# Optimization experiments

Measured on AMD Instinct MI355X. Metric: run time of the kernel, lower is better.

Reference implementation:

```python
import jax, jax.numpy as jnp
import numpy as np

H, HK, HD, WIN = 16, 4, 128, 512  # query heads, kv heads, head_dim, window
NEG = -1e30


def setup_inputs() -> dict:
    key = jax.random.key(0)
    ks = jax.random.split(key, 5)
    B, T, D = 2, 4096, 2048
    s = 1.0 / np.sqrt(D)
    return {
        "x": jax.random.normal(ks[0], (B, T, D), dtype=jnp.float32),
        "Wq": jax.random.normal(ks[1], (D, H * HD), dtype=jnp.float32) * s,
        "Wk": jax.random.normal(ks[2], (D, HK * HD), dtype=jnp.float32) * s,
        "Wv": jax.random.normal(ks[3], (D, HK * HD), dtype=jnp.float32) * s,
        "Wo": jax.random.normal(ks[4], (H * HD, D), dtype=jnp.float32) * s,
    }


def _local_attn(x, Wq, Wk, Wv, Wo):
    B, T, D = x.shape
    nrep = H // HK
    nb = T // WIN
    scale = 1.0 / np.sqrt(HD)

    q = (x @ Wq).reshape(B, nb, WIN, HK, nrep, HD)
    k = (x @ Wk).reshape(B, nb, WIN, HK, HD)
    v = (x @ Wv).reshape(B, nb, WIN, HK, HD)

    # each query block attends to its own block + the previous block,
    k_prev = jnp.concatenate([jnp.zeros_like(k[:, :1]), k[:, :-1]], axis=1)
    v_prev = jnp.concatenate([jnp.zeros_like(v[:, :1]), v[:, :-1]], axis=1)
    kcat = jnp.concatenate([k_prev, k], axis=2)  # [B,nb,2W,HK,HD]
    vcat = jnp.concatenate([v_prev, v], axis=2)

    r = jnp.arange(WIN)[:, None]       # query offset in block
    c = jnp.arange(2 * WIN)[None, :]   # key offset in concat window
    allowed = jnp.where(c < WIN, c > r, (c - WIN) <= r)  # [W,2W]
    first_block = (jnp.arange(nb) == 0)[:, None, None]   # block 0 has no prev
    allowed = allowed[None, :, :] & ~(first_block & (c < WIN)[None])  # [nb,W,2W]

    scores = jnp.einsum('bnqhrd,bnkhd->bnhrqk', q, kcat) * scale
    scores = jnp.where(allowed[None, :, None, None], scores, NEG)
    attn = jax.nn.softmax(scores, axis=-1)
    out = jnp.einsum('bnhrqk,bnkhd->bnqhrd', attn, vcat)
    out = out.reshape(B, T, H * HD)
    return out @ Wo


def reference(x, Wq, Wk, Wv, Wo):
    return _local_attn(x, Wq, Wk, Wv, Wo)
```

## Files before the change

kernel.cpp:

```cpp
#include <hip/hip_runtime.h>
#include <stdint.h>


typedef unsigned short u16;
typedef __attribute__((ext_vector_type(8))) short frag8;
typedef __attribute__((ext_vector_type(4))) float f32x4;

#define TILE 128

__device__ __forceinline__ u16 f2bf(float f) {
  union { float f; unsigned u; } c; c.f = f;
  unsigned u = c.u;
  return (u16)((u + 0x7fffu + ((u >> 16) & 1u)) >> 16);
}

__device__ __forceinline__ void async16(const u16* g, u16* l) {
  __builtin_amdgcn_global_load_lds((const __attribute__((address_space(1))) void*)g,
                                   (__attribute__((address_space(3))) void*)l, 16, 0, 0);
}

__device__ __forceinline__ void xcd_map(int& bx, int& by) {
  const int gx = gridDim.x;
  const int cx = gx >> 3;
  int id = blockIdx.y * gx + blockIdx.x;
  int xcd = id & 7, local = id >> 3;
  bx = xcd * cx + (local % cx);
  by = local / cx;
}

template <typename OutT>
__global__ __launch_bounds__(512, 2) void k_gemm256(const u16* __restrict__ A, int lda,
                                                    const u16* __restrict__ Bt, int ldb,
                                                    OutT* __restrict__ C, int ldc, int K,
                                                    float oscale) {
  __shared__ alignas(16) u16 Ab[2][256 * 64];
  __shared__ alignas(16) u16 Bb[2][256 * 64];
  const int tid = threadIdx.x, lane = tid & 63, wave = tid >> 6;
  const int wm = wave >> 2, wn = wave & 3;
  const int quad = lane >> 4, l16 = lane & 15;

  int bx, by;
  xcd_map(bx, by);

  const int rsub = wave * 8 + (lane >> 3);
  const int csub = ((lane & 7) ^ (lane >> 3)) * 8;
  const u16* Ag = A + ((long)bx * 256 + rsub) * lda + csub;
  const u16* Bg = Bt + ((long)by * 256 + rsub) * ldb + csub;
  const long a64 = (long)64 * lda, b64 = (long)64 * ldb;

  const int rsw = (l16 & 7) << 3;

  f32x4 acc[8][4];
#pragma unroll
  for (int i = 0; i < 8; ++i)
#pragma unroll
    for (int j = 0; j < 4; ++j) acc[i][j] = (f32x4){0.f, 0.f, 0.f, 0.f};

  const int nt = K >> 6;

#pragma unroll
  for (int c = 0; c < 4; ++c) {
    async16(Ag + c * a64, &Ab[0][c * 4096 + wave * 512]);
    async16(Bg + c * b64, &Bb[0][c * 4096 + wave * 512]);
  }

  for (int t = 0; t < nt; ++t) {
    const int buf = t & 1, nb = buf ^ 1;
    const long koff = (long)(t + 1) << 6;
    frag8 af[4][2], bf[2][2];

    if (t + 1 < nt) {
#pragma unroll
      for (int c = 0; c < 4; ++c) {
        async16(Ag + c * a64 + koff, &Ab[nb][c * 4096 + wave * 512]);
        async16(Bg + c * b64 + koff, &Bb[nb][c * 4096 + wave * 512]);
      }
      asm volatile("s_waitcnt vmcnt(8)" ::: "memory");
    } else {
      asm volatile("s_waitcnt vmcnt(0)" ::: "memory");
    }
    __builtin_amdgcn_s_barrier();
    asm volatile("" ::: "memory");

#pragma unroll
    for (int i = 0; i < 4; ++i)
#pragma unroll
      for (int kk = 0; kk < 2; ++kk)
        af[i][kk] = *(const frag8*)(&Ab[buf][(wm * 128 + i * 16 + l16) * 64 +
                                             ((kk * 32 + quad * 8) ^ rsw)]);
#pragma unroll
    for (int j = 0; j < 2; ++j)
#pragma unroll
      for (int kk = 0; kk < 2; ++kk)
        bf[j][kk] = *(const frag8*)(&Bb[buf][(wn * 64 + j * 16 + l16) * 64 +
                                             ((kk * 32 + quad * 8) ^ rsw)]);
    __builtin_amdgcn_s_setprio(1);
#pragma unroll
    for (int kk = 0; kk < 2; ++kk)
#pragma unroll
      for (int i = 0; i < 4; ++i)
#pragma unroll
        for (int j = 0; j < 2; ++j)
          acc[i][j] = __builtin_amdgcn_mfma_f32_16x16x32_bf16(af[i][kk], bf[j][kk], acc[i][j], 0, 0, 0);
    __builtin_amdgcn_s_setprio(0);
    __builtin_amdgcn_s_barrier();

#pragma unroll
    for (int j = 0; j < 2; ++j)
#pragma unroll
      for (int kk = 0; kk < 2; ++kk)
        bf[j][kk] = *(const frag8*)(&Bb[buf][(wn * 64 + (j + 2) * 16 + l16) * 64 +
                                             ((kk * 32 + quad * 8) ^ rsw)]);
    __builtin_amdgcn_s_setprio(1);
#pragma unroll
    for (int kk = 0; kk < 2; ++kk)
#pragma unroll
      for (int i = 0; i < 4; ++i)
#pragma unroll
        for (int j = 0; j < 2; ++j)
          acc[i][j + 2] = __builtin_amdgcn_mfma_f32_16x16x32_bf16(af[i][kk], bf[j][kk], acc[i][j + 2], 0, 0, 0);
    __builtin_amdgcn_s_setprio(0);
    __builtin_amdgcn_s_barrier();

#pragma unroll
    for (int i = 0; i < 4; ++i)
#pragma unroll
      for (int kk = 0; kk < 2; ++kk)
        af[i][kk] = *(const frag8*)(&Ab[buf][(wm * 128 + (i + 4) * 16 + l16) * 64 +
                                             ((kk * 32 + quad * 8) ^ rsw)]);
#pragma unroll
    for (int j = 0; j < 2; ++j)
#pragma unroll
      for (int kk = 0; kk < 2; ++kk)
        bf[j][kk] = *(const frag8*)(&Bb[buf][(wn * 64 + j * 16 + l16) * 64 +
                                             ((kk * 32 + quad * 8) ^ rsw)]);
    __builtin_amdgcn_s_setprio(1);
#pragma unroll
    for (int kk = 0; kk < 2; ++kk)
#pragma unroll
      for (int i = 0; i < 4; ++i)
#pragma unroll
        for (int j = 0; j < 2; ++j)
          acc[i + 4][j] = __builtin_amdgcn_mfma_f32_16x16x32_bf16(af[i][kk], bf[j][kk], acc[i + 4][j], 0, 0, 0);
    __builtin_amdgcn_s_setprio(0);
    __builtin_amdgcn_s_barrier();

#pragma unroll
    for (int j = 0; j < 2; ++j)
#pragma unroll
      for (int kk = 0; kk < 2; ++kk)
        bf[j][kk] = *(const frag8*)(&Bb[buf][(wn * 64 + (j + 2) * 16 + l16) * 64 +
                                             ((kk * 32 + quad * 8) ^ rsw)]);
    __builtin_amdgcn_s_setprio(1);
#pragma unroll
    for (int kk = 0; kk < 2; ++kk)
#pragma unroll
      for (int i = 0; i < 4; ++i)
#pragma unroll
        for (int j = 0; j < 2; ++j)
          acc[i + 4][j + 2] = __builtin_amdgcn_mfma_f32_16x16x32_bf16(af[i][kk], bf[j][kk], acc[i + 4][j + 2], 0, 0, 0);
    __builtin_amdgcn_s_setprio(0);
    __builtin_amdgcn_s_barrier();
  }

  OutT* Ct = C + ((long)bx * 256 + wm * 128) * ldc + (long)by * 256 + wn * 64;
#pragma unroll
  for (int i = 0; i < 8; ++i)
#pragma unroll
    for (int j = 0; j < 4; ++j) {
      int r0 = i * 16 + quad * 4, cc = j * 16 + l16;
#pragma unroll
      for (int r = 0; r < 4; ++r) {
        float v = acc[i][j][r] * oscale;
        if constexpr (sizeof(OutT) == 2)
          Ct[(long)(r0 + r) * ldc + cc] = f2bf(v);
        else
          Ct[(long)(r0 + r) * ldc + cc] = v;
      }
    }
}

__device__ __forceinline__ void gemm_core(const u16* __restrict__ A, int lda,
                                          const u16* __restrict__ Bt, int ldb,
                                          int K, u16* As, u16* Bs, f32x4 acc[4][4]) {
  const int tid = threadIdx.x;
  const int lane = tid & 63, wave = tid >> 6;
  const int wr = wave >> 1, wc = wave & 1;
  const int quad = lane >> 4, l16 = lane & 15;
#pragma unroll
  for (int i = 0; i < 4; ++i)
#pragma unroll
    for (int j = 0; j < 4; ++j) acc[i][j] = (f32x4){0.f, 0.f, 0.f, 0.f};

  const int row0 = tid >> 2, offc = (tid & 3) * 8;
  const int nt = K >> 5;

#pragma unroll
  for (int r = 0; r < 2; ++r) {
    int row = r * 64 + row0;
    async16(A + (long)row * lda + offc, As + r * 2048 + wave * 512);
    async16(Bt + (long)row * ldb + offc, Bs + r * 2048 + wave * 512);
  }

  for (int t = 0; t < nt; ++t) {
    const int bo = (t & 1) * 4096, nbo = bo ^ 4096;
    if (t + 1 < nt) {
      const int k0 = (t + 1) * 32;
#pragma unroll
      for (int r = 0; r < 2; ++r) {
        int row = r * 64 + row0;
        async16(A + (long)row * lda + k0 + offc, As + nbo + r * 2048 + wave * 512);
        async16(Bt + (long)row * ldb + k0 + offc, Bs + nbo + r * 2048 + wave * 512);
      }
      asm volatile("s_waitcnt vmcnt(4)" ::: "memory");
    } else {
      asm volatile("s_waitcnt vmcnt(0)" ::: "memory");
    }
    __builtin_amdgcn_s_barrier();
    asm volatile("" ::: "memory");

    frag8 af[4], bf[4];
#pragma unroll
    for (int i = 0; i < 4; ++i)
      af[i] = *(const frag8*)(As + bo + (wr * 64 + i * 16 + l16) * 32 + quad * 8);
#pragma unroll
    for (int j = 0; j < 4; ++j)
      bf[j] = *(const frag8*)(Bs + bo + (wc * 64 + j * 16 + l16) * 32 + quad * 8);
#pragma unroll
    for (int i = 0; i < 4; ++i)
#pragma unroll
      for (int j = 0; j < 4; ++j)
        acc[i][j] = __builtin_amdgcn_mfma_f32_16x16x32_bf16(af[i], bf[j], acc[i][j], 0, 0, 0);
    asm volatile("" ::: "memory");
    __builtin_amdgcn_s_barrier();
  }
}

#define EPI_COORDS                                             \
  const int lane = threadIdx.x & 63, wave = threadIdx.x >> 6;  \
  const int wr = wave >> 1, wc = wave & 1;                     \
  const int quad = lane >> 4, l16 = lane & 15;

__global__ __launch_bounds__(256) void k_gemm_bf16(const u16* __restrict__ A, int lda,
                                                   const u16* __restrict__ Bt, int ldb,
                                                   u16* __restrict__ C, int ldc, int K) {
  __shared__ alignas(16) u16 smem[4 * TILE * 32];
  int bx, by; xcd_map(bx, by);
  f32x4 acc[4][4];
  gemm_core(A + (long)bx * TILE * lda, lda,
            Bt + (long)by * TILE * ldb, ldb, K, smem, smem + 2 * TILE * 32, acc);
  EPI_COORDS
  u16* Ct = C + (long)bx * TILE * ldc + (long)by * TILE;
#pragma unroll
  for (int i = 0; i < 4; ++i)
#pragma unroll
    for (int j = 0; j < 4; ++j) {
      int r0 = wr * 64 + i * 16 + quad * 4, cc = wc * 64 + j * 16 + l16;
#pragma unroll
      for (int r = 0; r < 4; ++r) Ct[(long)(r0 + r) * ldc + cc] = f2bf(acc[i][j][r]);
    }
}

__global__ __launch_bounds__(256) void k_gemm_bf16t(const u16* __restrict__ A, int lda,
                                                    const u16* __restrict__ Bt, int ldb,
                                                    u16* __restrict__ Ct, int ldct, int K) {
  __shared__ alignas(16) u16 smem[4 * TILE * 32];
  int bx, by; xcd_map(bx, by);
  f32x4 acc[4][4];
  gemm_core(A + (long)bx * TILE * lda, lda,
            Bt + (long)by * TILE * ldb, ldb, K, smem, smem + 2 * TILE * 32, acc);
  EPI_COORDS
  u16* Cb = Ct + (long)by * TILE * ldct + (long)bx * TILE;
#pragma unroll
  for (int i = 0; i < 4; ++i)
#pragma unroll
    for (int j = 0; j < 4; ++j) {
      int n = wc * 64 + j * 16 + l16, m0 = wr * 64 + i * 16 + quad * 4;
      ushort4 o;
      o.x = f2bf(acc[i][j][0]); o.y = f2bf(acc[i][j][1]);
      o.z = f2bf(acc[i][j][2]); o.w = f2bf(acc[i][j][3]);
      *(ushort4*)(Cb + (long)n * ldct + m0) = o;
    }
}

__global__ __launch_bounds__(256, 2) void k_attn(const u16* __restrict__ qb,
                                                 const u16* __restrict__ kb,
                                                 const u16* __restrict__ vT,
                                                 u16* __restrict__ O) {
  __shared__ alignas(16) u16 Ks[2][64 * 128];
  __shared__ alignas(16) u16 Vs[2][128 * 64];
  const int tid = threadIdx.x, lane = tid & 63, wave = tid >> 6;
  const int quad = lane >> 4, l16 = lane & 15;

  const int id = blockIdx.x + 4 * blockIdx.y + 32 * blockIdx.z;
  const int g = (id & 7) | ((id >> 7) << 3);
  const int w = (id >> 3) & 15;
  const int hk = g & 3, blk = (g >> 2) & 7, b = g >> 5;
  const int h = hk * 4 + (w & 3), qi = w >> 2;

  const long tok_q = (long)b * 4096 + blk * 512 + qi * 128;

  frag8 qf[2][4];
#pragma unroll
  for (int i = 0; i < 2; ++i)
#pragma unroll
    for (int kt = 0; kt < 4; ++kt)
      qf[i][kt] = *(const frag8*)(qb + (tok_q + wave * 32 + i * 16 + l16) * 2048 +
                                  h * 128 + kt * 32 + quad * 8);

  f32x4 o_acc[2][8];
  float m_r[2][4], l_r[2][4];
#pragma unroll
  for (int i = 0; i < 2; ++i) {
#pragma unroll
    for (int j = 0; j < 8; ++j) o_acc[i][j] = (f32x4){0.f, 0.f, 0.f, 0.f};
#pragma unroll
    for (int r = 0; r < 4; ++r) { m_r[i][r] = -1e30f; l_r[i][r] = 0.f; }
  }

  const int rsw = (l16 & 7) << 3;

  auto stage = [&](int buf, int ci) {
    const long tk = (long)b * 4096 + (blk - 1) * 512 + ci * 64;
#pragma unroll
    for (int c = 0; c < 4; ++c) {
      const int idx = (wave * 4 + c) * 512 + lane * 8;
      {
        int row = idx >> 7, col = idx & 127;
        async16(kb + (tk + row) * 512 + hk * 128 + (col ^ ((row & 7) << 3)),
                &Ks[buf][(wave * 4 + c) * 512]);
      }
      {
        int row = idx >> 6, col = idx & 63;
        async16(vT + ((long)hk * 128 + row) * 8192 + tk + (col ^ ((row & 7) << 3)),
                &Vs[buf][(wave * 4 + c) * 512]);
      }
    }
  };

  const int c0 = blk ? 2 * qi : 8, c1 = 9 + 2 * qi;
  int cur = 0;
  stage(0, c0);
  asm volatile("s_waitcnt vmcnt(0)" ::: "memory");
  __builtin_amdgcn_s_barrier();
  asm volatile("" ::: "memory");

  for (int ci = c0; ci <= c1; ++ci) {
    if (ci < c1) stage(cur ^ 1, ci + 1);

    f32x4 s_acc[2][4];
#pragma unroll
    for (int i = 0; i < 2; ++i)
#pragma unroll
      for (int j = 0; j < 4; ++j) s_acc[i][j] = (f32x4){0.f, 0.f, 0.f, 0.f};
#pragma unroll
    for (int kt = 0; kt < 4; ++kt) {
      frag8 bfr[4];
#pragma unroll
      for (int j = 0; j < 4; ++j)
        bfr[j] = *(const frag8*)(&Ks[cur][(j * 16 + l16) * 128 + ((kt * 32 + quad * 8) ^ rsw)]);
#pragma unroll
      for (int i = 0; i < 2; ++i)
#pragma unroll
        for (int j = 0; j < 4; ++j)
          s_acc[i][j] = __builtin_amdgcn_mfma_f32_16x16x32_bf16(qf[i][kt], bfr[j], s_acc[i][j], 0, 0, 0);
    }

    const bool prev = (ci < 8);
    const int doff = (prev ? ci * 64 : (ci - 8) * 64) - qi * 128;
    float mc[2][4];
#pragma unroll
    for (int i = 0; i < 2; ++i)
#pragma unroll
      for (int r = 0; r < 4; ++r) mc[i][r] = -1e30f;
#pragma unroll
    for (int i = 0; i < 2; ++i)
#pragma unroll
      for (int j = 0; j < 4; ++j)
#pragma unroll
        for (int r = 0; r < 4; ++r) {
          int rl = wave * 32 + i * 16 + quad * 4 + r;
          int lk = j * 16 + l16;
          bool ok = prev ? (lk + doff > rl) : (lk + doff <= rl);
          float s = ok ? s_acc[i][j][r] : -1e30f;
          s_acc[i][j][r] = s;
          mc[i][r] = fmaxf(mc[i][r], s);
        }
#pragma unroll
    for (int o = 1; o < 16; o <<= 1)
#pragma unroll
      for (int i = 0; i < 2; ++i)
#pragma unroll
        for (int r = 0; r < 4; ++r)
          mc[i][r] = fmaxf(mc[i][r], __shfl_xor(mc[i][r], o));

    bool need = false;
#pragma unroll
    for (int i = 0; i < 2; ++i)
#pragma unroll
      for (int r = 0; r < 4; ++r) need = need || (mc[i][r] > m_r[i][r] + 8.f);
    if (__any(need)) {
      float alpha[2][4];
#pragma unroll
      for (int i = 0; i < 2; ++i)
#pragma unroll
        for (int r = 0; r < 4; ++r) {
          float mn = fmaxf(m_r[i][r], mc[i][r]);
          alpha[i][r] = __expf(m_r[i][r] - mn);
          m_r[i][r] = mn;
          l_r[i][r] *= alpha[i][r];
        }
#pragma unroll
      for (int i = 0; i < 2; ++i)
#pragma unroll
        for (int j = 0; j < 8; ++j)
#pragma unroll
          for (int r = 0; r < 4; ++r) o_acc[i][j][r] *= alpha[i][r];
    }

    float ps[2][4];
#pragma unroll
    for (int i = 0; i < 2; ++i)
#pragma unroll
      for (int r = 0; r < 4; ++r) ps[i][r] = 0.f;
#pragma unroll
    for (int i = 0; i < 2; ++i)
#pragma unroll
      for (int j = 0; j < 4; ++j)
#pragma unroll
        for (int r = 0; r < 4; ++r) {
          float s = s_acc[i][j][r];
          float e = __expf(s - m_r[i][r]);
          e = (s == -1e30f) ? 0.f : e;
          s_acc[i][j][r] = e;
          ps[i][r] += e;
        }
#pragma unroll
    for (int o = 1; o < 16; o <<= 1)
#pragma unroll
      for (int i = 0; i < 2; ++i)
#pragma unroll
        for (int r = 0; r < 4; ++r) ps[i][r] += __shfl_xor(ps[i][r], o);
#pragma unroll
    for (int i = 0; i < 2; ++i)
#pragma unroll
      for (int r = 0; r < 4; ++r) l_r[i][r] += ps[i][r];

    asm volatile("" ::: "memory");
    __builtin_amdgcn_s_barrier();
    asm volatile("" ::: "memory");

    u16* PsW = &Ks[cur][wave * 2048];
#pragma unroll
    for (int i = 0; i < 2; ++i)
#pragma unroll
      for (int r = 0; r < 4; ++r) {
        int xw = ((quad * 4 + r) & 7) << 3;
#pragma unroll
        for (int j = 0; j < 4; ++j)
          PsW[(i * 16 + quad * 4 + r) * 64 + ((j * 16 + l16) ^ xw)] = f2bf(s_acc[i][j][r]);
      }

#pragma unroll
    for (int kt = 0; kt < 2; ++kt) {
      frag8 pf[2], vf[8];
#pragma unroll
      for (int i = 0; i < 2; ++i)
        pf[i] = *(const frag8*)(PsW + (i * 16 + l16) * 64 + ((kt * 32 + quad * 8) ^ rsw));
#pragma unroll
      for (int j = 0; j < 8; ++j)
        vf[j] = *(const frag8*)(&Vs[cur][(j * 16 + l16) * 64 + ((kt * 32 + quad * 8) ^ rsw)]);
#pragma unroll
      for (int i = 0; i < 2; ++i)
#pragma unroll
        for (int j = 0; j < 8; ++j)
          o_acc[i][j] = __builtin_amdgcn_mfma_f32_16x16x32_bf16(pf[i], vf[j], o_acc[i][j], 0, 0, 0);
    }

    asm volatile("s_waitcnt vmcnt(0)" ::: "memory");
    __builtin_amdgcn_s_barrier();
    asm volatile("" ::: "memory");
    cur ^= 1;
  }

  float inv[2][4];
#pragma unroll
  for (int i = 0; i < 2; ++i)
#pragma unroll
    for (int r = 0; r < 4; ++r) inv[i][r] = 1.0f / l_r[i][r];
  u16* Ob = &Ks[0][0];
#pragma unroll
  for (int i = 0; i < 2; ++i)
#pragma unroll
    for (int j = 0; j < 8; ++j)
#pragma unroll
      for (int r = 0; r < 4; ++r)
        Ob[(wave * 32 + i * 16 + quad * 4 + r) * 128 + j * 16 + l16] =
            f2bf(o_acc[i][j][r] * inv[i][r]);
  __syncthreads();
#pragma unroll
  for (int p = 0; p < 8; ++p) {
    int idx = p * 256 + tid;
    int row = idx >> 4, col = (idx & 15) * 8;
    *(frag8*)(O + (tok_q + row) * 2048 + h * 128 + col) = *(const frag8*)(Ob + row * 128 + col);
  }
}

__global__ void k_convert(const float4* __restrict__ x, ushort4* __restrict__ xb) {
  int i = blockIdx.x * 256 + threadIdx.x;
  float4 f = x[i];
  ushort4 o;
  o.x = f2bf(f.x); o.y = f2bf(f.y); o.z = f2bf(f.z); o.w = f2bf(f.w);
  xb[i] = o;
}

__global__ void k_transpose(const float* __restrict__ W, u16* __restrict__ WT, int K, int N) {
  __shared__ float sh[32][33];
  int n0 = blockIdx.x * 32, k0 = blockIdx.y * 32;
  int tx = threadIdx.x, ty = threadIdx.y;
#pragma unroll
  for (int i = 0; i < 32; i += 8) sh[ty + i][tx] = W[(long)(k0 + ty + i) * N + n0 + tx];
  __syncthreads();
#pragma unroll
  for (int i = 0; i < 32; i += 8) WT[(long)(n0 + ty + i) * K + k0 + tx] = f2bf(sh[tx][ty + i]);
}

extern "C" void kernel_launch(void* const* d_in, const int* in_sizes, int n_in,
                              void* d_out, int out_size, void* d_ws, size_t ws_size,
                              hipStream_t stream) {
  const float* x  = (const float*)d_in[0];
  const float* Wq = (const float*)d_in[1];
  const float* Wk = (const float*)d_in[2];
  const float* Wv = (const float*)d_in[3];
  const float* Wo = (const float*)d_in[4];
  float* out = (float*)d_out;

  const long BT = 8192, D = 2048, NKV = 512;
  size_t off = 0;
  auto alloc = [&](size_t bytes) -> char* {
    off = (off + 255) & ~(size_t)255;
    char* p = (char*)d_ws + off;
    off += bytes;
    return p;
  };

  u16* xb  = (u16*)alloc((size_t)BT * D * 2);
  u16* WqT = (u16*)alloc((size_t)D * D * 2);
  u16* WkT = (u16*)alloc((size_t)NKV * D * 2);
  u16* WvT = (u16*)alloc((size_t)NKV * D * 2);
  u16* WoT = (u16*)alloc((size_t)D * D * 2);
  u16* qb  = (u16*)alloc((size_t)BT * D * 2);
  u16* kb  = (u16*)alloc((size_t)BT * NKV * 2);
  u16* vT  = (u16*)alloc((size_t)NKV * BT * 2);
  u16* Oa  = xb;

  k_convert<<<16384, 256, 0, stream>>>((const float4*)x, (ushort4*)xb);
  dim3 tb(32, 8);
  k_transpose<<<dim3(64, 64), tb, 0, stream>>>(Wq, WqT, 2048, 2048);
  k_transpose<<<dim3(16, 64), tb, 0, stream>>>(Wk, WkT, 2048, 512);
  k_transpose<<<dim3(16, 64), tb, 0, stream>>>(Wv, WvT, 2048, 512);
  k_transpose<<<dim3(64, 64), tb, 0, stream>>>(Wo, WoT, 2048, 2048);

  k_gemm256<u16><<<dim3(32, 8), 512, 0, stream>>>(xb, 2048, WqT, 2048, qb, 2048, 2048,
                                                  0.08838834764831845f);
  k_gemm_bf16 <<<dim3(64, 4),  256, 0, stream>>>(xb, 2048, WkT, 2048, kb, 512, 2048);
  k_gemm_bf16t<<<dim3(64, 4),  256, 0, stream>>>(xb, 2048, WvT, 2048, vT, 8192, 2048);

  k_attn<<<dim3(4, 8, 32), 256, 0, stream>>>(qb, kb, vT, Oa);

  k_gemm256<float><<<dim3(32, 8), 512, 0, stream>>>(Oa, 2048, WoT, 2048, out, 2048, 2048,
                                                    1.0f);
}
```

Measured before the change: 459.2 us.

## Single-buffer V tile, raise attention occupancy, skip unneeded masking, use exp2

The attention kernel keeps K double-buffered but gives V a single LDS buffer, loaded one iteration late. This frees LDS so launch bounds can go from two to three blocks per CU, and fine-grained vmcnt waits replace full drains. Masking is skipped for chunks that lie wholly inside the allowed region. Softmax uses raw v_exp_f32 (exp2), with log2(e) folded into the Q projection scale. The cost is extra barriers and tighter register budgets that could cause spills.

Result: slower. 545.2 us (+18.7%).

```diff
diff --git a/kernel.cpp b/kernel.cpp
--- a/kernel.cpp
+++ b/kernel.cpp
@@ -12,6 +12,12 @@
   union { float f; unsigned u; } c; c.f = f;
   unsigned u = c.u;
   return (u16)((u + 0x7fffu + ((u >> 16) & 1u)) >> 16);
+}
+
+__device__ __forceinline__ float fexp2(float x) {
+  float r;
+  asm("v_exp_f32 %0, %1" : "=v"(r) : "v"(x));
+  return r;
 }
 
 __device__ __forceinline__ void async16(const u16* g, u16* l) {
@@ -283,12 +289,12 @@
     }
 }
 
-__global__ __launch_bounds__(256, 2) void k_attn(const u16* __restrict__ qb,
+__global__ __launch_bounds__(256, 3) void k_attn(const u16* __restrict__ qb,
                                                  const u16* __restrict__ kb,
                                                  const u16* __restrict__ vT,
                                                  u16* __restrict__ O) {
   __shared__ alignas(16) u16 Ks[2][64 * 128];
-  __shared__ alignas(16) u16 Vs[2][128 * 64];
+  __shared__ alignas(16) u16 Vs[128 * 64];
   const int tid = threadIdx.x, lane = tid & 63, wave = tid >> 6;
   const int quad = lane >> 4, l16 = lane & 15;
 
@@ -320,33 +326,45 @@
 
   const int rsw = (l16 & 7) << 3;
 
-  auto stage = [&](int buf, int ci) {
+  auto stageK = [&](int buf, int ci) {
     const long tk = (long)b * 4096 + (blk - 1) * 512 + ci * 64;
 #pragma unroll
     for (int c = 0; c < 4; ++c) {
       const int idx = (wave * 4 + c) * 512 + lane * 8;
-      {
-        int row = idx >> 7, col = idx & 127;
-        async16(kb + (tk + row) * 512 + hk * 128 + (col ^ ((row & 7) << 3)),
-                &Ks[buf][(wave * 4 + c) * 512]);
-      }
-      {
-        int row = idx >> 6, col = idx & 63;
-        async16(vT + ((long)hk * 128 + row) * 8192 + tk + (col ^ ((row & 7) << 3)),
-                &Vs[buf][(wave * 4 + c) * 512]);
-      }
+      int row = idx >> 7, col = idx & 127;
+      async16(kb + (tk + row) * 512 + hk * 128 + (col ^ ((row & 7) << 3)),
+              &Ks[buf][(wave * 4 + c) * 512]);
+    }
+  };
+  auto stageV = [&](int ci) {
+    const long tk = (long)b * 4096 + (blk - 1) * 512 + ci * 64;
+#pragma unroll
+    for (int c = 0; c < 4; ++c) {
+      const int idx = (wave * 4 + c) * 512 + lane * 8;
+      int row = idx >> 6, col = idx & 63;
+      async16(vT + ((long)hk * 128 + row) * 8192 + tk + (col ^ ((row & 7) << 3)),
+              &Vs[(wave * 4 + c) * 512]);
     }
   };
 
   const int c0 = blk ? 2 * qi : 8, c1 = 9 + 2 * qi;
   int cur = 0;
-  stage(0, c0);
+  stageK(0, c0);
+  stageV(c0);
   asm volatile("s_waitcnt vmcnt(0)" ::: "memory");
   __builtin_amdgcn_s_barrier();
   asm volatile("" ::: "memory");
 
   for (int ci = c0; ci <= c1; ++ci) {
-    if (ci < c1) stage(cur ^ 1, ci + 1);
+    if (ci > c0) stageV(ci);
+    if (ci < c1) {
+      stageK(cur ^ 1, ci + 1);
+      asm volatile("s_waitcnt vmcnt(8)" ::: "memory");
+    } else {
+      asm volatile("s_waitcnt vmcnt(4)" ::: "memory");
+    }
+    __builtin_amdgcn_s_barrier();
+    asm volatile("" ::: "memory");
 
     f32x4 s_acc[2][4];
 #pragma unroll
@@ -373,19 +391,28 @@
     for (int i = 0; i < 2; ++i)
 #pragma unroll
       for (int r = 0; r < 4; ++r) mc[i][r] = -1e30f;
-#pragma unroll
-    for (int i = 0; i < 2; ++i)
-#pragma unroll
-      for (int j = 0; j < 4; ++j)
-#pragma unroll
-        for (int r = 0; r < 4; ++r) {
-          int rl = wave * 32 + i * 16 + quad * 4 + r;
-          int lk = j * 16 + l16;
-          bool ok = prev ? (lk + doff > rl) : (lk + doff <= rl);
-          float s = ok ? s_acc[i][j][r] : -1e30f;
-          s_acc[i][j][r] = s;
-          mc[i][r] = fmaxf(mc[i][r], s);
-        }
+    if (doff >= 0 && doff <= 64) {
+#pragma unroll
+      for (int i = 0; i < 2; ++i)
+#pragma unroll
+        for (int j = 0; j < 4; ++j)
+#pragma unroll
+          for (int r = 0; r < 4; ++r) {
+            int rl = wave * 32 + i * 16 + quad * 4 + r;
+            int lk = j * 16 + l16;
+            bool ok = prev ? (lk + doff > rl) : (lk + doff <= rl);
+            float s = ok ? s_acc[i][j][r] : -1e30f;
+            s_acc[i][j][r] = s;
+            mc[i][r] = fmaxf(mc[i][r], s);
+          }
+    } else {
+#pragma unroll
+      for (int i = 0; i < 2; ++i)
+#pragma unroll
+        for (int j = 0; j < 4; ++j)
+#pragma unroll
+          for (int r = 0; r < 4; ++r) mc[i][r] = fmaxf(mc[i][r], s_acc[i][j][r]);
+    }
 #pragma unroll
     for (int o = 1; o < 16; o <<= 1)
 #pragma unroll
@@ -406,7 +433,7 @@
 #pragma unroll
         for (int r = 0; r < 4; ++r) {
           float mn = fmaxf(m_r[i][r], mc[i][r]);
-          alpha[i][r] = __expf(m_r[i][r] - mn);
+          alpha[i][r] = fexp2(m_r[i][r] - mn);
           m_r[i][r] = mn;
           l_r[i][r] *= alpha[i][r];
         }
@@ -430,7 +457,7 @@
 #pragma unroll
         for (int r = 0; r < 4; ++r) {
           float s = s_acc[i][j][r];
-          float e = __expf(s - m_r[i][r]);
+          float e = fexp2(s - m_r[i][r]);
           e = (s == -1e30f) ? 0.f : e;
           s_acc[i][j][r] = e;
           ps[i][r] += e;
@@ -446,7 +473,10 @@
 #pragma unroll
       for (int r = 0; r < 4; ++r) l_r[i][r] += ps[i][r];
 
-    asm volatile("" ::: "memory");
+    if (ci < c1)
+      asm volatile("s_waitcnt vmcnt(4)" ::: "memory");
+    else
+      asm volatile("s_waitcnt vmcnt(0)" ::: "memory");
     __builtin_amdgcn_s_barrier();
     asm volatile("" ::: "memory");
 
@@ -469,7 +499,7 @@
         pf[i] = *(const frag8*)(PsW + (i * 16 + l16) * 64 + ((kt * 32 + quad * 8) ^ rsw));
 #pragma unroll
       for (int j = 0; j < 8; ++j)
-        vf[j] = *(const frag8*)(&Vs[cur][(j * 16 + l16) * 64 + ((kt * 32 + quad * 8) ^ rsw)]);
+        vf[j] = *(const frag8*)(&Vs[(j * 16 + l16) * 64 + ((kt * 32 + quad * 8) ^ rsw)]);
 #pragma unroll
       for (int i = 0; i < 2; ++i)
 #pragma unroll
@@ -477,7 +507,7 @@
           o_acc[i][j] = __builtin_amdgcn_mfma_f32_16x16x32_bf16(pf[i], vf[j], o_acc[i][j], 0, 0, 0);
     }
 
-    asm volatile("s_waitcnt vmcnt(0)" ::: "memory");
+    asm volatile("" ::: "memory");
     __builtin_amdgcn_s_barrier();
     asm volatile("" ::: "memory");
     cur ^= 1;
@@ -561,8 +591,9 @@
   k_transpose<<<dim3(16, 64), tb, 0, stream>>>(Wv, WvT, 2048, 512);
   k_transpose<<<dim3(64, 64), tb, 0, stream>>>(Wo, WoT, 2048, 2048);
 
+  const float qscale = 0.08838834764831845f * 1.4426950408889634f;
   k_gemm256<u16><<<dim3(32, 8), 512, 0, stream>>>(xb, 2048, WqT, 2048, qb, 2048, 2048,
-                                                  0.08838834764831845f);
+                                                  qscale);
   k_gemm_bf16 <<<dim3(64, 4),  256, 0, stream>>>(xb, 2048, WkT, 2048, kb, 512, 2048);
   k_gemm_bf16t<<<dim3(64, 4),  256, 0, stream>>>(xb, 2048, WvT, 2048, vT, 8192, 2048);
 
```
